# Performance work log

Measured on AMD Instinct MI355X. Metric: run time of the kernel, lower is better.

Reference implementation:

```python
import jax, jax.numpy as jnp
import numpy as np

N_NODES = 50000
N_EDGES = 1_250_000
D_IN = 64
D_OUT = 64


def setup_inputs() -> dict:
    key = jax.random.key(0)
    k1, k2, k3, k4, k5 = jax.random.split(key, 5)
    feature = jax.random.normal(k1, (N_NODES, D_IN), dtype=jnp.float32)
    src = jax.random.randint(k2, (N_EDGES,), 0, N_NODES, dtype=jnp.int32)
    dst = jax.random.randint(k3, (N_EDGES,), 0, N_NODES, dtype=jnp.int32)
    W = jax.random.normal(k4, (D_OUT, D_IN), dtype=jnp.float32) * (1.0 / np.sqrt(D_IN))
    b = jax.random.normal(k5, (D_OUT,), dtype=jnp.float32) * 0.01
    return {"feature": feature, "src": src, "dst": dst, "W": W, "b": b}


def reference(feature, src, dst, W, b):
    # copy_u + sum: for each edge, message = feature[src]; reduce-sum at dst.
    msgs = feature[src]                                  # [E, D_IN] irregular gather
    h = jax.ops.segment_sum(msgs, dst, num_segments=N_NODES)  # [N, D_IN] scatter-add
    return h @ W.T + b                                   # nn.Linear
```

## Files before the change

kernel.cpp:

```cpp
#include <hip/hip_runtime.h>

#define D 64
#define SNB 256
#define CVB 192
#define NBP 1024
#define SCAP 5120
#define SLOTN 2048
#define NSTR 120
#define GPAD 16
#define SCAN_CHUNK 1024

typedef float v2f __attribute__((ext_vector_type(2)));

static __device__ __forceinline__ unsigned short f2bf(float f) {
    unsigned u = __float_as_uint(f);
    unsigned r = (u + 0x7FFFu + ((u >> 16) & 1u)) >> 16;
    return (unsigned short)r;
}

__global__ void __launch_bounds__(1024)
build5_kernel(const int* __restrict__ src, const int* __restrict__ dst,
              int* __restrict__ gcur, unsigned* __restrict__ pairs,
              const float* __restrict__ feature, const float* __restrict__ W,
              unsigned short* __restrict__ fw,
              int n_edges, int nb, int chunk, int n_nodes) {
    if (blockIdx.x >= SNB) {
        __shared__ float4 Wt4c[64 * 16];
        __shared__ float  Fs[64 * 68];
        int tid = threadIdx.x;

        if (blockIdx.x == SNB && tid < 16) {
            ushort4 z; z.x = z.y = z.z = z.w = 0;
            ((ushort4*)(fw + (size_t)n_nodes * D))[tid] = z;
        }
        {
            int k = tid >> 4, oq = tid & 15;
            float4 v;
            v.x = W[(4 * oq + 0) * 64 + k];
            v.y = W[(4 * oq + 1) * 64 + k];
            v.z = W[(4 * oq + 2) * 64 + k];
            v.w = W[(4 * oq + 3) * 64 + k];
            Wt4c[k * 16 + oq] = v;
        }
        int r = tid >> 4, c4 = tid & 15;
        for (int t = blockIdx.x - SNB; t < nb; t += CVB) {
            int n = t * 64 + r;
            int nc = (n < n_nodes) ? n : 0;
            float4 fv = ((const float4*)(feature + (size_t)nc * 64))[c4];
            __syncthreads();
            Fs[r * 68 + c4 * 4 + 0] = fv.x;
            Fs[r * 68 + c4 * 4 + 1] = fv.y;
            Fs[r * 68 + c4 * 4 + 2] = fv.z;
            Fs[r * 68 + c4 * 4 + 3] = fv.w;
            __syncthreads();
            v2f acc01 = {0.f, 0.f}, acc23 = {0.f, 0.f};
#pragma unroll
            for (int k = 0; k < 64; ++k) {
                float f = Fs[r * 68 + k];
                float4 wv = Wt4c[k * 16 + c4];
                v2f w01; w01.x = wv.x; w01.y = wv.y;
                v2f w23; w23.x = wv.z; w23.y = wv.w;
                acc01 += w01 * f;
                acc23 += w23 * f;
            }
            if (n < n_nodes) {
                ushort4 o;
                o.x = f2bf(acc01.x); o.y = f2bf(acc01.y);
                o.z = f2bf(acc23.x); o.w = f2bf(acc23.y);
                ((ushort4*)(fw + (size_t)n * D))[c4] = o;
            }
        }
        return;
    }

    __shared__ unsigned inb[SCAP];
    __shared__ int hist[NBP];
    __shared__ int gpos[NBP];

    int blk = blockIdx.x, tid = threadIdx.x;

    for (int i = tid; i < NBP; i += 1024) hist[i] = 0;
    __syncthreads();

    int e0 = blk * chunk;
    int e1 = e0 + chunk; if (e1 > n_edges) e1 = n_edges;
    int m = e1 - e0;

    for (int i = tid; i < m; i += 1024) {
        int d_ = dst[e0 + i];
        int s_ = src[e0 + i];
        inb[i] = ((unsigned)(d_ >> 6) << 22) | ((unsigned)(d_ & 63) << 16) | (unsigned)s_;
        atomicAdd(&hist[d_ >> 6], 1);
    }
    __syncthreads();

    if (tid < nb) {
        int v = hist[tid];
        if (v > 0) {
            int gb = atomicAdd(&gcur[tid * GPAD], v);
            gpos[tid] = (gb + v <= SLOTN) ? (tid * SLOTN + gb) : (int)0x80000000;
        } else {
            gpos[tid] = (int)0x80000000;
        }
    }
    __syncthreads();

    for (int i = tid; i < m; i += 1024) {
        unsigned p = inb[i];
        int pos = atomicAdd(&gpos[p >> 22], 1);
        if (pos >= 0) pairs[pos] = p & 0x3FFFFFu;
    }
}

__global__ void __launch_bounds__(512, 8)
agg9_kernel(const unsigned short* __restrict__ fw,
            const unsigned* __restrict__ pairs,
            const int* __restrict__ gcur,
            const float* __restrict__ bias,
            float* __restrict__ out, int n_nodes) {
    __shared__ unsigned short slist[64 * NSTR];
    __shared__ int cur[64];

    int tid = threadIdx.x;
    int bkt = blockIdx.x;
    int len = gcur[bkt * GPAD]; if (len > SLOTN) len = SLOTN;
    int e0 = bkt * SLOTN;

    {
        unsigned short zs = (unsigned short)n_nodes;
        unsigned zp = ((unsigned)zs << 16) | (unsigned)zs;
        unsigned* s4 = (unsigned*)slist;
        for (int i = tid; i < (64 * NSTR) / 2; i += 512) s4[i] = zp;
        if (tid < 64) cur[tid] = 0;
    }
    __syncthreads();

    for (int i = tid; i < len; i += 512) {
        unsigned p = pairs[e0 + i];
        int ln = (p >> 16) & 63;
        int pos = atomicAdd(&cur[ln], 1);
        if (pos < NSTR) slist[ln * NSTR + pos] = (unsigned short)(p & 0xffffu);
    }
    __syncthreads();

    int lane = tid & 63, w = tid >> 6;
    int h  = lane >> 5;
    int g  = (lane >> 3) & 3;
    int sl = lane & 7;

    float4 b0 = *(const float4*)(bias + sl * 8);
    float4 b1 = *(const float4*)(bias + sl * 8 + 4);
    const unsigned short* fwp = fw + sl * 8;

    for (int qq = 0; qq < 4; ++qq) {
        int ln = w * 8 + qq * 2 + h;
        int d = cur[ln]; if (d > NSTR) d = NSTR;
        { int dx = __shfl_xor(d, 32, 64); if (dx > d) d = dx; }
        int off = ln * NSTR;

        v2f a0 = {0.f, 0.f}, a1 = {0.f, 0.f}, a2 = {0.f, 0.f}, a3 = {0.f, 0.f};

        for (int j = 0; j < d; j += 8) {
            int s0 = slist[off + j + g];
            int s1 = slist[off + j + 4 + g];
            uint4 v0 = *(const uint4*)(fwp + s0 * D);
            uint4 v1 = *(const uint4*)(fwp + s1 * D);
            v2f t;
            t.x = __uint_as_float(v0.x << 16);
            t.y = __uint_as_float(v0.x & 0xffff0000u);  a0 += t;
            t.x = __uint_as_float(v0.y << 16);
            t.y = __uint_as_float(v0.y & 0xffff0000u);  a1 += t;
            t.x = __uint_as_float(v0.z << 16);
            t.y = __uint_as_float(v0.z & 0xffff0000u);  a2 += t;
            t.x = __uint_as_float(v0.w << 16);
            t.y = __uint_as_float(v0.w & 0xffff0000u);  a3 += t;
            t.x = __uint_as_float(v1.x << 16);
            t.y = __uint_as_float(v1.x & 0xffff0000u);  a0 += t;
            t.x = __uint_as_float(v1.y << 16);
            t.y = __uint_as_float(v1.y & 0xffff0000u);  a1 += t;
            t.x = __uint_as_float(v1.z << 16);
            t.y = __uint_as_float(v1.z & 0xffff0000u);  a2 += t;
            t.x = __uint_as_float(v1.w << 16);
            t.y = __uint_as_float(v1.w & 0xffff0000u);  a3 += t;
        }

        a0.x += __shfl_xor(a0.x, 8, 64);  a0.y += __shfl_xor(a0.y, 8, 64);
        a1.x += __shfl_xor(a1.x, 8, 64);  a1.y += __shfl_xor(a1.y, 8, 64);
        a2.x += __shfl_xor(a2.x, 8, 64);  a2.y += __shfl_xor(a2.y, 8, 64);
        a3.x += __shfl_xor(a3.x, 8, 64);  a3.y += __shfl_xor(a3.y, 8, 64);
        a0.x += __shfl_xor(a0.x, 16, 64); a0.y += __shfl_xor(a0.y, 16, 64);
        a1.x += __shfl_xor(a1.x, 16, 64); a1.y += __shfl_xor(a1.y, 16, 64);
        a2.x += __shfl_xor(a2.x, 16, 64); a2.y += __shfl_xor(a2.y, 16, 64);
        a3.x += __shfl_xor(a3.x, 16, 64); a3.y += __shfl_xor(a3.y, 16, 64);

        if (g == 0) {
            int n = bkt * 64 + ln;
            if (n < n_nodes) {
                float4 r0, r1;
                r0.x = a0.x + b0.x; r0.y = a0.y + b0.y;
                r0.z = a1.x + b0.z; r0.w = a1.y + b0.w;
                r1.x = a2.x + b1.x; r1.y = a2.y + b1.y;
                r1.z = a3.x + b1.z; r1.w = a3.y + b1.w;
                *(float4*)(out + n * D + sl * 8)     = r0;
                *(float4*)(out + n * D + sl * 8 + 4) = r1;
            }
        }
    }
}


__global__ void hist_kernel(const int* __restrict__ dst, int* __restrict__ counts, int n_edges) {
    int e = blockIdx.x * blockDim.x + threadIdx.x;
    if (e < n_edges) atomicAdd(&counts[dst[e]], 1);
}

__global__ void reduce_kernel(const int* __restrict__ counts, int* __restrict__ partials, int n_nodes) {
    __shared__ int wsums[4];
    int tid = threadIdx.x;
    int base = blockIdx.x * SCAN_CHUNK + tid * 4;
    int s = 0;
#pragma unroll
    for (int i = 0; i < 4; ++i) {
        int idx = base + i;
        if (idx < n_nodes) s += counts[idx];
    }
    for (int o = 32; o > 0; o >>= 1) s += __shfl_down(s, o, 64);
    int lane = tid & 63, wave = tid >> 6;
    if (lane == 0) wsums[wave] = s;
    __syncthreads();
    if (tid == 0) partials[blockIdx.x] = wsums[0] + wsums[1] + wsums[2] + wsums[3];
}

__global__ void scan_partials_kernel(const int* __restrict__ partials, int* __restrict__ pscan, int nblk) {
    int lane = threadIdx.x;
    int v = (lane < nblk) ? partials[lane] : 0;
    int orig = v;
    for (int o = 1; o < 64; o <<= 1) {
        int y = __shfl_up(v, o, 64);
        if (lane >= o) v += y;
    }
    if (lane < nblk) pscan[lane] = v - orig;
}

__global__ void scan_kernel(const int* __restrict__ counts, const int* __restrict__ pscan,
                            int* __restrict__ offsets, int* __restrict__ cursors, int n_nodes) {
    __shared__ int wsums[4];
    int tid = threadIdx.x;
    int base = blockIdx.x * SCAN_CHUNK + tid * 4;
    int c[4];
    int tsum = 0;
#pragma unroll
    for (int i = 0; i < 4; ++i) {
        int idx = base + i;
        c[i] = (idx < n_nodes) ? counts[idx] : 0;
        tsum += c[i];
    }
    int lane = tid & 63, wave = tid >> 6;
    int x = tsum;
    for (int o = 1; o < 64; o <<= 1) {
        int y = __shfl_up(x, o, 64);
        if (lane >= o) x += y;
    }
    if (lane == 63) wsums[wave] = x;
    __syncthreads();
    int wpre = 0;
    for (int w = 0; w < wave; ++w) wpre += wsums[w];
    int excl = (x - tsum) + wpre + pscan[blockIdx.x];
#pragma unroll
    for (int i = 0; i < 4; ++i) {
        int idx = base + i;
        if (idx < n_nodes) { offsets[idx] = excl; cursors[idx] = excl; }
        excl += c[i];
    }
}

__global__ void fill_kernel(const int* __restrict__ src, const int* __restrict__ dst,
                            int* __restrict__ cursors, int* __restrict__ elist, int n_edges) {
    int e = blockIdx.x * blockDim.x + threadIdx.x;
    if (e < n_edges) {
        int pos = atomicAdd(&cursors[dst[e]], 1);
        elist[pos] = src[e];
    }
}

__global__ void agg_linear_kernel(const float* __restrict__ feature,
                                  const int* __restrict__ elist,
                                  const int* __restrict__ offsets,
                                  const int* __restrict__ counts,
                                  const float* __restrict__ W,
                                  const float* __restrict__ b,
                                  float* __restrict__ out,
                                  int n_nodes, int total_waves) {
    __shared__ float Wt[64 * 65];
    int tid = threadIdx.x;
    for (int i = tid; i < 64 * 64; i += 256) {
        int o = i >> 6, k = i & 63;
        Wt[k * 65 + o] = W[i];
    }
    __syncthreads();
    int lane = tid & 63;
    int waveId = (blockIdx.x * 256 + tid) >> 6;
    float bias = b[lane];
    for (int n = waveId; n < n_nodes; n += total_waves) {
        int off = offsets[n];
        int deg = counts[n];
        float acc = 0.f;
        int j = 0;
        for (; j + 4 <= deg; j += 4) {
            int s0 = elist[off + j + 0];
            int s1 = elist[off + j + 1];
            int s2 = elist[off + j + 2];
            int s3 = elist[off + j + 3];
            acc += feature[s0 * D + lane] + feature[s1 * D + lane]
                 + feature[s2 * D + lane] + feature[s3 * D + lane];
        }
        for (; j < deg; ++j) acc += feature[elist[off + j] * D + lane];
        float r = bias;
#pragma unroll
        for (int k = 0; k < 64; ++k) r += __shfl(acc, k, 64) * Wt[k * 65 + lane];
        out[n * D + lane] = r;
    }
}

__global__ void gcn_scatter_kernel(const float* __restrict__ feature,
                                   const int* __restrict__ src,
                                   const int* __restrict__ dst,
                                   float* __restrict__ out,
                                   int n_edges) {
    int e = blockIdx.x * 4 + (threadIdx.x >> 6);
    int lane = threadIdx.x & 63;
    if (e < n_edges) atomicAdd(&out[dst[e] * D + lane], feature[src[e] * D + lane]);
}

__global__ void gcn_linear_kernel(float* __restrict__ out,
                                  const float* __restrict__ W,
                                  const float* __restrict__ b,
                                  int n_nodes) {
    __shared__ float Wt[64 * 65];
    int tid = threadIdx.x;
    for (int i = tid; i < 64 * 64; i += 256) {
        int o = i >> 6, k = i & 63;
        Wt[k * 65 + o] = W[i];
    }
    __syncthreads();
    int lane = tid & 63;
    int n = blockIdx.x * 4 + (tid >> 6);
    if (n >= n_nodes) return;
    float val = out[n * D + lane];
    float acc = b[lane];
#pragma unroll
    for (int k = 0; k < 64; ++k) acc += __shfl(val, k, 64) * Wt[k * 65 + lane];
    out[n * D + lane] = acc;
}


extern "C" void kernel_launch(void* const* d_in, const int* in_sizes, int n_in,
                              void* d_out, int out_size, void* d_ws, size_t ws_size,
                              hipStream_t stream) {
    const float* feature = (const float*)d_in[0];
    const int* src       = (const int*)d_in[1];
    const int* dst       = (const int*)d_in[2];
    const float* W       = (const float*)d_in[3];
    const float* b       = (const float*)d_in[4];
    float* out           = (float*)d_out;

    int n_edges = in_sizes[1];
    int n_nodes = in_sizes[0] / D;

    int nb = (n_nodes + 63) >> 6;
    int chunk = (n_edges + SNB - 1) / SNB;

    size_t pairsWords = (size_t)nb * SLOTN;
    size_t needA = (size_t)NBP * GPAD * sizeof(int) + pairsWords * sizeof(int)
                 + (size_t)(n_nodes + 1) * D * sizeof(unsigned short);

    if (n_nodes <= 65535 && nb <= NBP && chunk <= SCAP && ws_size >= needA) {
        int* gcur          = (int*)d_ws;
        unsigned* pairs    = (unsigned*)(gcur + (size_t)NBP * GPAD);
        unsigned short* fw = (unsigned short*)(pairs + pairsWords);

        hipMemsetAsync(gcur, 0, (size_t)NBP * GPAD * sizeof(int), stream);
        build5_kernel<<<SNB + CVB, 1024, 0, stream>>>(src, dst, gcur, pairs,
                                                      feature, W, fw,
                                                      n_edges, nb, chunk, n_nodes);
        agg9_kernel<<<nb, 512, 0, stream>>>(fw, pairs, gcur, b, out, n_nodes);
        return;
    }

    size_t needB = ((size_t)3 * n_nodes + 128 + (size_t)n_edges) * sizeof(int);
    int nblk_scan = (n_nodes + SCAN_CHUNK - 1) / SCAN_CHUNK;
    if (ws_size >= needB && nblk_scan <= 64) {
        int* counts   = (int*)d_ws;
        int* offsets  = counts + n_nodes;
        int* cursors  = offsets + n_nodes;
        int* partials = cursors + n_nodes;
        int* pscan    = partials + 64;
        int* elist    = pscan + 64;

        hipMemsetAsync(counts, 0, (size_t)n_nodes * sizeof(int), stream);
        hist_kernel<<<(n_edges + 255) / 256, 256, 0, stream>>>(dst, counts, n_edges);
        reduce_kernel<<<nblk_scan, 256, 0, stream>>>(counts, partials, n_nodes);
        scan_partials_kernel<<<1, 64, 0, stream>>>(partials, pscan, nblk_scan);
        scan_kernel<<<nblk_scan, 256, 0, stream>>>(counts, pscan, offsets, cursors, n_nodes);
        fill_kernel<<<(n_edges + 255) / 256, 256, 0, stream>>>(src, dst, cursors, elist, n_edges);
        agg_linear_kernel<<<3125, 256, 0, stream>>>(feature, elist, offsets, counts, W, b, out,
                                                    n_nodes, 3125 * 4);
        return;
    }

    hipMemsetAsync(d_out, 0, (size_t)out_size * sizeof(float), stream);
    gcn_scatter_kernel<<<(n_edges + 3) / 4, 256, 0, stream>>>(feature, src, dst, out, n_edges);
    gcn_linear_kernel<<<(n_nodes + 3) / 4, 256, 0, stream>>>(out, W, b, n_nodes);
}
```

Measured before the change: 121.5 us.

## Locally sort edges by bucket before global write; unroll gather loop wider

The build kernel now runs a block-wide prefix scan over per-bucket counts, sorts its edge chunk into a second shared buffer grouped by bucket, and writes pairs to global memory in sorted order with a per-bucket delta. The goal is contiguous, coalesced global stores in place of scattered atomic-indexed writes. Shared memory is merged into one aliased buffer to fit the extra staging array. The aggregation kernel pads per-node lists to 128 and processes 16 neighbours per iteration for more memory-level parallelism, at the cost of more registers and possibly more padded zero-row loads.

New measurement: 119.5 us. No clear change (-1.7%).

```diff
diff --git a/kernel.cpp b/kernel.cpp
--- a/kernel.cpp
+++ b/kernel.cpp
@@ -6,7 +6,7 @@
 #define NBP 1024
 #define SCAP 5120
 #define SLOTN 2048
-#define NSTR 120
+#define NSTR 128
 #define GPAD 16
 #define SCAN_CHUNK 1024
 
@@ -19,14 +19,16 @@
 }
 
 __global__ void __launch_bounds__(1024)
-build5_kernel(const int* __restrict__ src, const int* __restrict__ dst,
+build6_kernel(const int* __restrict__ src, const int* __restrict__ dst,
               int* __restrict__ gcur, unsigned* __restrict__ pairs,
               const float* __restrict__ feature, const float* __restrict__ W,
               unsigned short* __restrict__ fw,
               int n_edges, int nb, int chunk, int n_nodes) {
+    __shared__ float4 smem4[3076];
+
     if (blockIdx.x >= SNB) {
-        __shared__ float4 Wt4c[64 * 16];
-        __shared__ float  Fs[64 * 68];
+        float4* Wt4c = smem4;
+        float*  Fs   = (float*)(smem4 + 1024);
         int tid = threadIdx.x;
 
         if (blockIdx.x == SNB && tid < 16) {
@@ -73,9 +75,11 @@
         return;
     }
 
-    __shared__ unsigned inb[SCAP];
-    __shared__ int hist[NBP];
-    __shared__ int gpos[NBP];
+    unsigned* inb  = (unsigned*)smem4;
+    unsigned* inb2 = inb + SCAP;
+    int* hist      = (int*)(inb2 + SCAP);
+    int* delta     = hist + NBP;
+    int* wsums     = delta + NBP;
 
     int blk = blockIdx.x, tid = threadIdx.x;
 
@@ -94,30 +98,55 @@
     }
     __syncthreads();
 
-    if (tid < nb) {
-        int v = hist[tid];
-        if (v > 0) {
-            int gb = atomicAdd(&gcur[tid * GPAD], v);
-            gpos[tid] = (gb + v <= SLOTN) ? (tid * SLOTN + gb) : (int)0x80000000;
-        } else {
-            gpos[tid] = (int)0x80000000;
-        }
-    }
+    int lane = tid & 63, wv = tid >> 6;
+    int v = hist[tid];
+    int x = v;
+    for (int o = 1; o < 64; o <<= 1) {
+        int y = __shfl_up(x, o, 64);
+        if (lane >= o) x += y;
+    }
+    if (lane == 63) wsums[wv] = x;
+    __syncthreads();
+    if (tid < 16) {
+        int s = wsums[tid], xx = s;
+        for (int o = 1; o < 16; o <<= 1) {
+            int y = __shfl_up(xx, o, 64);
+            if (tid >= o) xx += y;
+        }
+        wsums[tid] = xx - s;
+    }
+    __syncthreads();
+    int epre = x - v + wsums[wv];
+
+    int dlt = (int)0x80000000;
+    if (tid < nb && v > 0) {
+        int gb = atomicAdd(&gcur[tid * GPAD], v);
+        if (gb + v <= SLOTN) dlt = tid * SLOTN + gb - epre;
+    }
+    delta[tid] = dlt;
+    hist[tid] = epre;
     __syncthreads();
 
     for (int i = tid; i < m; i += 1024) {
         unsigned p = inb[i];
-        int pos = atomicAdd(&gpos[p >> 22], 1);
-        if (pos >= 0) pairs[pos] = p & 0x3FFFFFu;
+        int pos = atomicAdd(&hist[p >> 22], 1);
+        inb2[pos] = p;
+    }
+    __syncthreads();
+
+    for (int i = tid; i < m; i += 1024) {
+        unsigned p = inb2[i];
+        int a = delta[p >> 22] + i;
+        if (a >= 0) pairs[a] = p & 0x3FFFFFu;
     }
 }
 
 __global__ void __launch_bounds__(512, 8)
-agg9_kernel(const unsigned short* __restrict__ fw,
-            const unsigned* __restrict__ pairs,
-            const int* __restrict__ gcur,
-            const float* __restrict__ bias,
-            float* __restrict__ out, int n_nodes) {
+agg10_kernel(const unsigned short* __restrict__ fw,
+             const unsigned* __restrict__ pairs,
+             const int* __restrict__ gcur,
+             const float* __restrict__ bias,
+             float* __restrict__ out, int n_nodes) {
     __shared__ unsigned short slist[64 * NSTR];
     __shared__ int cur[64];
 
@@ -160,11 +189,15 @@
 
         v2f a0 = {0.f, 0.f}, a1 = {0.f, 0.f}, a2 = {0.f, 0.f}, a3 = {0.f, 0.f};
 
-        for (int j = 0; j < d; j += 8) {
+        for (int j = 0; j < d; j += 16) {
             int s0 = slist[off + j + g];
             int s1 = slist[off + j + 4 + g];
+            int s2 = slist[off + j + 8 + g];
+            int s3 = slist[off + j + 12 + g];
             uint4 v0 = *(const uint4*)(fwp + s0 * D);
             uint4 v1 = *(const uint4*)(fwp + s1 * D);
+            uint4 v2 = *(const uint4*)(fwp + s2 * D);
+            uint4 v3 = *(const uint4*)(fwp + s3 * D);
             v2f t;
             t.x = __uint_as_float(v0.x << 16);
             t.y = __uint_as_float(v0.x & 0xffff0000u);  a0 += t;
@@ -182,6 +215,22 @@
             t.y = __uint_as_float(v1.z & 0xffff0000u);  a2 += t;
             t.x = __uint_as_float(v1.w << 16);
             t.y = __uint_as_float(v1.w & 0xffff0000u);  a3 += t;
+            t.x = __uint_as_float(v2.x << 16);
+            t.y = __uint_as_float(v2.x & 0xffff0000u);  a0 += t;
+            t.x = __uint_as_float(v2.y << 16);
+            t.y = __uint_as_float(v2.y & 0xffff0000u);  a1 += t;
+            t.x = __uint_as_float(v2.z << 16);
+            t.y = __uint_as_float(v2.z & 0xffff0000u);  a2 += t;
+            t.x = __uint_as_float(v2.w << 16);
+            t.y = __uint_as_float(v2.w & 0xffff0000u);  a3 += t;
+            t.x = __uint_as_float(v3.x << 16);
+            t.y = __uint_as_float(v3.x & 0xffff0000u);  a0 += t;
+            t.x = __uint_as_float(v3.y << 16);
+            t.y = __uint_as_float(v3.y & 0xffff0000u);  a1 += t;
+            t.x = __uint_as_float(v3.z << 16);
+            t.y = __uint_as_float(v3.z & 0xffff0000u);  a2 += t;
+            t.x = __uint_as_float(v3.w << 16);
+            t.y = __uint_as_float(v3.w & 0xffff0000u);  a3 += t;
         }
 
         a0.x += __shfl_xor(a0.x, 8, 64);  a0.y += __shfl_xor(a0.y, 8, 64);
@@ -380,10 +429,10 @@
         unsigned short* fw = (unsigned short*)(pairs + pairsWords);
 
         hipMemsetAsync(gcur, 0, (size_t)NBP * GPAD * sizeof(int), stream);
-        build5_kernel<<<SNB + CVB, 1024, 0, stream>>>(src, dst, gcur, pairs,
+        build6_kernel<<<SNB + CVB, 1024, 0, stream>>>(src, dst, gcur, pairs,
                                                       feature, W, fw,
                                                       n_edges, nb, chunk, n_nodes);
-        agg9_kernel<<<nb, 512, 0, stream>>>(fw, pairs, gcur, b, out, n_nodes);
+        agg10_kernel<<<nb, 512, 0, stream>>>(fw, pairs, gcur, b, out, n_nodes);
         return;
     }
 
```
